# Kernel optimization log

Measured on AMD Instinct MI355X. Metric: run time of the kernel, lower is better.

## Reference

```python
import jax, jax.numpy as jnp
import numpy as np

N_NODES = 50000
N_EDGES = 800000
D = 128          # input_node_dim == output_node_dim (residual)
T = 3            # number of node types == number of edge types
NODE_IN = D + T * D  # node updater input dim = 512


def setup_inputs() -> dict:
    key = jax.random.key(0)
    ks = jax.random.split(key, 8)
    scale = 0.05
    return {
        "node_feature": jax.random.normal(ks[0], (N_NODES, D), jnp.float32),
        "W_e": jax.random.normal(ks[1], (T, D, D), jnp.float32) * scale,
        "b_e": jnp.zeros((T, D), jnp.float32),
        "W_n": jax.random.normal(ks[2], (T, D, NODE_IN), jnp.float32) * scale,
        "b_n": jnp.zeros((T, D), jnp.float32),
        "edge_src": jax.random.randint(ks[3], (N_EDGES,), 0, N_NODES, jnp.int32),
        "edge_dst": jax.random.randint(ks[4], (N_EDGES,), 0, N_NODES, jnp.int32),
        "edge_type": jax.random.randint(ks[5], (N_EDGES,), 0, T, jnp.int32),
        "node_type": jax.random.randint(ks[6], (N_NODES,), 0, T, jnp.int32),
    }


def reference(node_feature, W_e, b_e, W_n, b_n, edge_src, edge_dst, edge_type, node_type):
    N, Din = node_feature.shape
    n_types = W_e.shape[0]
    out_dim = W_e.shape[1]

    # message_function: per-edge-type MLP on source features, relu, zero elsewhere
    src = node_feature[edge_src]                      # [E, D] gather
    parts = [jax.nn.relu(node_feature)]               # reduce_function relu's node_feature
    for t in range(n_types):
        msg = jax.nn.relu(src @ W_e[t].T + b_e[t])    # [E, out]
        msg = jnp.where((edge_type == t)[:, None], msg, jnp.zeros((), msg.dtype))
        # mailbox sum over incoming edges per destination node
        parts.append(jax.ops.segment_sum(msg, edge_dst, num_segments=N))
    agg = jnp.concatenate(parts, axis=1)              # [N, D + T*out]

    # per-node-type updater MLP, dispatched by node_type
    updated = jnp.zeros((N, out_dim), node_feature.dtype)
    for t in range(n_types):
        o = agg @ W_n[t].T + b_n[t]                   # [N, out]
        updated = jnp.where((node_type == t)[:, None], o, updated)

    # use_residual = True
    return updated + node_feature
```

## Files before the change

kernel.cpp:

```cpp
#include <hip/hip_runtime.h>
#include <hip/hip_bf16.h>

#define NN 50000
#define NE 800000
#define DD 128
#define NT 3
#define AGGW 384
#define EM 64
#define EM2 128
#define LDK 136
#define CB 32
#define LDK2 520
#define NBITS 7
#define NBINS ((NN + 127) / 128)
#define EPB 8192
#define BINCAP 2560
#define NTILES_MAX (((NN + EM - 1) / EM) + NT)
#define NTILE_PAD (((NTILES_MAX + 7) / 8) * 8)

typedef __bf16 bf16x8 __attribute__((ext_vector_type(8)));
typedef float f32x4 __attribute__((ext_vector_type(4)));
typedef unsigned short u16x8 __attribute__((ext_vector_type(8)));
typedef unsigned int u32x4 __attribute__((ext_vector_type(4)));

__device__ __forceinline__ unsigned short f2b(float f) {
    __hip_bfloat16 h = __float2bfloat16(f);
    return __builtin_bit_cast(unsigned short, h);
}
__device__ __forceinline__ float b2f(unsigned int u16bits) {
    unsigned int x = u16bits << 16;
    return __builtin_bit_cast(float, x);
}

__global__ void k_prep(const float* __restrict__ nf, const float* __restrict__ We,
                       const float* __restrict__ Wn, unsigned short* __restrict__ nfb,
                       unsigned short* __restrict__ Web, unsigned short* __restrict__ Wnb,
                       int* __restrict__ bhist, int* __restrict__ cnts) {
    size_t i = (size_t)blockIdx.x * blockDim.x + threadIdx.x;
    if (i < NBINS) bhist[i] = 0;
    if (i >= NBINS && i < NBINS + 16) cnts[i - NBINS] = 0;
    const size_t n0 = (size_t)NN * DD / 8;
    const size_t n1 = (size_t)NT * DD * DD / 8;
    const size_t n2 = (size_t)NT * DD * 512 / 8;
    size_t total = n0 + n1 + n2;
    for (size_t p = i; p < total; p += (size_t)gridDim.x * blockDim.x) {
        const float* s; unsigned short* d; size_t off;
        if (p < n0)            { s = nf; d = nfb; off = p; }
        else if (p < n0 + n1)  { s = We; d = Web; off = p - n0; }
        else                   { s = Wn; d = Wnb; off = p - n0 - n1; }
        const float4* f4 = (const float4*)(s + off * 8);
        float4 x = f4[0], y = f4[1];
        u16x8 u = { f2b(x.x), f2b(x.y), f2b(x.z), f2b(x.w),
                    f2b(y.x), f2b(y.y), f2b(y.z), f2b(y.w) };
        *(u16x8*)(d + off * 8) = u;
    }
}

__global__ __launch_bounds__(256) void k_binhist(const int* __restrict__ edst,
        const int* __restrict__ ntp, int* __restrict__ bhist, int* __restrict__ cnts) {
    __shared__ int lh[NBINS];
    __shared__ int ln[3];
    int tid = threadIdx.x;
    for (int i = tid; i < NBINS; i += 256) lh[i] = 0;
    if (tid < 3) ln[tid] = 0;
    __syncthreads();
    int i0 = blockIdx.x * blockDim.x + tid;
    int stride = gridDim.x * blockDim.x;
    for (int p = i0; p < NE; p += stride) atomicAdd(&lh[edst[p] >> NBITS], 1);
    for (int p = i0; p < NN; p += stride) atomicAdd(&ln[ntp[p]], 1);
    __syncthreads();
    for (int i = tid; i < NBINS; i += 256) if (lh[i]) atomicAdd(&bhist[i], lh[i]);
    if (tid < 3) atomicAdd(&cnts[6 + tid], ln[tid]);
}

__global__ __launch_bounds__(512) void k_binscan(const int* __restrict__ bhist,
        int* __restrict__ binptr, int* __restrict__ bincur, int* __restrict__ rowptr) {
    __shared__ int sa[NBINS], sb[NBINS];
    int tid = threadIdx.x;
    if (tid < NBINS) sa[tid] = bhist[tid];
    __syncthreads();
    int flip = 0;
    for (int off = 1; off < NBINS; off <<= 1) {
        int* src = flip ? sb : sa;
        int* dst = flip ? sa : sb;
        if (tid < NBINS) dst[tid] = src[tid] + ((tid >= off) ? src[tid - off] : 0);
        __syncthreads();
        flip ^= 1;
    }
    int* inc = flip ? sb : sa;
    if (tid < NBINS) {
        int excl = (tid == 0) ? 0 : inc[tid - 1];
        binptr[tid] = excl;
        bincur[tid] = excl;
    }
    if (tid == 0) { binptr[NBINS] = NE; rowptr[NN] = NE; }
}

__global__ __launch_bounds__(512) void k_mid(
        const unsigned short* __restrict__ nfb, const unsigned short* __restrict__ Web,
        const float* __restrict__ be, unsigned short* __restrict__ M,
        const int* __restrict__ esrc, const int* __restrict__ edst,
        const int* __restrict__ et, const int* __restrict__ ntp,
        int* __restrict__ bincur, int* __restrict__ cnts,
        int* __restrict__ pe, int* __restrict__ sn, int* __restrict__ rnk) {
    const int NEB = (NE + EPB - 1) / EPB;
    const int NCH2 = (NN + 511) / 512;
    const int TILES = (NN + EM2 - 1) / EM2;
    __shared__ unsigned short Wsm[DD][LDK];
    int tid = threadIdx.x, b = blockIdx.x;

    if (b < NEB) {
        int* lh = (int*)&Wsm[0][0];
        int* gb = lh + NBINS;
        int* lr = gb + NBINS;
        for (int i = tid; i < NBINS; i += 512) { lh[i] = 0; lr[i] = 0; }
        __syncthreads();
        int e0 = b * EPB;
#pragma unroll
        for (int i = 0; i < EPB; i += 512) {
            int e = e0 + i + tid;
            if (e < NE) atomicAdd(&lh[edst[e] >> NBITS], 1);
        }
        __syncthreads();
        for (int i = tid; i < NBINS; i += 512)
            if (lh[i]) gb[i] = atomicAdd(&bincur[i], lh[i]);
        __syncthreads();
#pragma unroll
        for (int i = 0; i < EPB; i += 512) {
            int e = e0 + i + tid;
            if (e < NE) {
                int d = edst[e];
                int t = et[e];
                int bin = d >> NBITS;
                int rank = atomicAdd(&lr[bin], 1);
                pe[gb[bin] + rank] = (t * NN + esrc[e]) | ((d & 127) << 18) | (t << 25);
            }
        }
    } else if (b < NEB + NCH2) {
        int* lcnt = (int*)&Wsm[0][0];
        int* lbase = lcnt + 4;
        if (tid < 3) lcnt[tid] = 0;
        __syncthreads();
        int p = (b - NEB) * 512 + tid;
        int t = -1, rank = 0;
        if (p < NN) { t = ntp[p]; rank = atomicAdd(&lcnt[t], 1); }
        __syncthreads();
        if (tid < 3) lbase[tid] = atomicAdd(&cnts[9 + tid], lcnt[tid]);
        __syncthreads();
        if (p < NN) {
            int c0 = cnts[6], c1 = cnts[7];
            int off = (t == 0) ? 0 : (t == 1) ? c0 : c0 + c1;
            int pos = off + lbase[t] + rank;
            sn[pos] = p;
            rnk[p] = pos;
        }
    } else {
        int bb = b - NEB - NCH2;
        int t = bb / TILES, tile = bb % TILES;
        int base = tile * EM2;
        int m = min(EM2, NN - base);
        {
            int row = tid >> 2, c0 = (tid & 3) * 32;
            const u16x8* src = (const u16x8*)(Web + ((size_t)t * DD + row) * DD + c0);
#pragma unroll
            for (int v = 0; v < 4; ++v) *(u16x8*)&Wsm[row][c0 + v * 8] = src[v];
        }
        __syncthreads();

        int wave = tid >> 6, l = tid & 63, lr2 = l & 15, kg = l >> 4;
        int arow = min(base + wave * 16 + lr2, NN - 1);
        const u16x8* Arow = (const u16x8*)(nfb + (size_t)arow * DD);
        f32x4 acc[8];
#pragma unroll
        for (int n = 0; n < 8; n++) acc[n] = (f32x4){0.f, 0.f, 0.f, 0.f};
#pragma unroll
        for (int k0 = 0; k0 < DD; k0 += 32) {
            bf16x8 a = __builtin_bit_cast(bf16x8, Arow[(k0 >> 3) + kg]);
#pragma unroll
            for (int n = 0; n < 8; n++) {
                bf16x8 bbv = *(const bf16x8*)&Wsm[n * 16 + lr2][k0 + kg * 8];
                acc[n] = __builtin_amdgcn_mfma_f32_16x16x32_bf16(a, bbv, acc[n], 0, 0, 0);
            }
        }
        unsigned short* Mt = M + (size_t)t * NN * DD;
#pragma unroll
        for (int n = 0; n < 8; n++) {
            int col = n * 16 + lr2;
            float bias = be[t * DD + col];
#pragma unroll
            for (int r = 0; r < 4; r++) {
                int row = wave * 16 + kg * 4 + r;
                if (row < m) {
                    float v = acc[n][r] + bias;
                    Mt[(size_t)(base + row) * DD + col] = f2b(fmaxf(v, 0.f));
                }
            }
        }
    }
}

__global__ __launch_bounds__(512) void k_binsort(const int* __restrict__ binptr,
        int* __restrict__ pe, int* __restrict__ rowptr) {
    __shared__ int lcnt[128], lrk[128], lrp[128];
    __shared__ unsigned int sorted[BINCAP];
    int b = blockIdx.x, tid = threadIdx.x;
    int beg = binptr[b], end = binptr[b + 1];
    int cnt = min(end - beg, BINCAP);
    if (tid < 128) { lcnt[tid] = 0; lrk[tid] = 0; }
    __syncthreads();
    for (int e = tid; e < cnt; e += 512)
        atomicAdd(&lcnt[(pe[beg + e] >> 18) & 127], 1);
    __syncthreads();
    if (tid < 64) {
        int v = lcnt[2 * tid] + lcnt[2 * tid + 1];
        int s = v;
        for (int d = 1; d < 64; d <<= 1) {
            int u = __shfl_up(s, d);
            if (tid >= d) s += u;
        }
        int excl = s - v;
        lrp[2 * tid] = excl;
        lrp[2 * tid + 1] = excl + lcnt[2 * tid];
    }
    __syncthreads();
    if (tid < 128) {
        int node = b * 128 + tid;
        if (node < NN) rowptr[node] = beg + lrp[tid];
    }
    for (int e = tid; e < cnt; e += 512) {
        unsigned int p = pe[beg + e];
        int d = (p >> 18) & 127;
        int pos = lrp[d] + atomicAdd(&lrk[d], 1);
        sorted[pos] = p;
    }
    __syncthreads();
    for (int e = tid; e < cnt; e += 512) pe[beg + e] = sorted[e];
}

__global__ __launch_bounds__(128) void k_agg(const unsigned short* __restrict__ M,
        const int* __restrict__ rowptr, const int* __restrict__ pe,
        const int* __restrict__ rnk, unsigned short* __restrict__ aggb) {
    int node = blockIdx.x * 8 + (threadIdx.x >> 4);
    int q = threadIdx.x & 15;
    int beg = rowptr[node], end = rowptr[node + 1];
    const u32x4* Mu4 = (const u32x4*)M;
    float a0[8] = {0,0,0,0,0,0,0,0};
    float a1[8] = {0,0,0,0,0,0,0,0};
    float a2[8] = {0,0,0,0,0,0,0,0};
    int e = beg;
    while (e < end) {
        unsigned int p[8];
        u32x4 v[8];
#pragma unroll
        for (int j = 0; j < 8; ++j) p[j] = pe[min(e + j, end - 1)];
#pragma unroll
        for (int j = 0; j < 8; ++j)
            if (e + j < end) v[j] = Mu4[(size_t)(p[j] & 0x3FFFFu) * 16 + q];
#pragma unroll
        for (int j = 0; j < 8; ++j) {
            if (e + j < end) {
                int t = p[j] >> 25;
                float f0 = b2f(v[j][0] & 0xFFFF), f1 = b2f(v[j][0] >> 16);
                float f2 = b2f(v[j][1] & 0xFFFF), f3 = b2f(v[j][1] >> 16);
                float f4 = b2f(v[j][2] & 0xFFFF), f5 = b2f(v[j][2] >> 16);
                float f6 = b2f(v[j][3] & 0xFFFF), f7 = b2f(v[j][3] >> 16);
                if (t == 0) {
                    a0[0] += f0; a0[1] += f1; a0[2] += f2; a0[3] += f3;
                    a0[4] += f4; a0[5] += f5; a0[6] += f6; a0[7] += f7;
                } else if (t == 1) {
                    a1[0] += f0; a1[1] += f1; a1[2] += f2; a1[3] += f3;
                    a1[4] += f4; a1[5] += f5; a1[6] += f6; a1[7] += f7;
                } else {
                    a2[0] += f0; a2[1] += f1; a2[2] += f2; a2[3] += f3;
                    a2[4] += f4; a2[5] += f5; a2[6] += f6; a2[7] += f7;
                }
            }
        }
        e += 8;
    }
    unsigned int* dst = (unsigned int*)(aggb + (size_t)rnk[node] * AGGW);
    u32x4 o0 = { (unsigned int)f2b(a0[0]) | ((unsigned int)f2b(a0[1]) << 16),
                 (unsigned int)f2b(a0[2]) | ((unsigned int)f2b(a0[3]) << 16),
                 (unsigned int)f2b(a0[4]) | ((unsigned int)f2b(a0[5]) << 16),
                 (unsigned int)f2b(a0[6]) | ((unsigned int)f2b(a0[7]) << 16) };
    u32x4 o1 = { (unsigned int)f2b(a1[0]) | ((unsigned int)f2b(a1[1]) << 16),
                 (unsigned int)f2b(a1[2]) | ((unsigned int)f2b(a1[3]) << 16),
                 (unsigned int)f2b(a1[4]) | ((unsigned int)f2b(a1[5]) << 16),
                 (unsigned int)f2b(a1[6]) | ((unsigned int)f2b(a1[7]) << 16) };
    u32x4 o2 = { (unsigned int)f2b(a2[0]) | ((unsigned int)f2b(a2[1]) << 16),
                 (unsigned int)f2b(a2[2]) | ((unsigned int)f2b(a2[3]) << 16),
                 (unsigned int)f2b(a2[4]) | ((unsigned int)f2b(a2[5]) << 16),
                 (unsigned int)f2b(a2[6]) | ((unsigned int)f2b(a2[7]) << 16) };
    ((u32x4*)dst)[q]        = o0;
    ((u32x4*)(dst + 64))[q] = o1;
    ((u32x4*)(dst + 128))[q] = o2;
}

__global__ __launch_bounds__(256, 3) void k_node(const float* __restrict__ nf,
        const unsigned short* __restrict__ nfb, const unsigned short* __restrict__ Wnb,
        const float* __restrict__ bn, const int* __restrict__ sn,
        const int* __restrict__ cnts, const unsigned short* __restrict__ aggb,
        float* __restrict__ out) {
    __shared__ unsigned short Wsm[CB][LDK2];
    int c0 = cnts[6], c1 = cnts[7], c2 = cnts[8];
    int n0 = (c0 + EM - 1) / EM, n1 = (c1 + EM - 1) / EM, n2 = (c2 + EM - 1) / EM;
    int ntile = n0 + n1 + n2;
    int b = blockIdx.x;
    int rt = (b & 7) * (NTILE_PAD / 8) + (b >> 3);
    if (rt >= ntile) return;
    int tid = threadIdx.x;
    int wave = tid >> 6, l = tid & 63, lr = l & 15, kg = l >> 4;
    int t, tile;
    if (rt < n0) { t = 0; tile = rt; }
    else if (rt < n0 + n1) { t = 1; tile = rt - n0; }
    else { t = 2; tile = rt - n0 - n1; }
    int off = (t == 0) ? 0 : (t == 1) ? c0 : c0 + c1;
    int cntt = (t == 0) ? c0 : (t == 1) ? c1 : c2;
    int base = off + tile * EM;
    int m = min(EM, cntt - tile * EM);

    int srtrow = base + min(wave * 16 + lr, m - 1);
    int myrow = sn[srtrow];
    const u16x8* An = (const u16x8*)(nfb + (size_t)myrow * DD);
    const u16x8* Ag = (const u16x8*)(aggb + (size_t)srtrow * AGGW);
    u16x8 afr[16];
#pragma unroll
    for (int kc = 0; kc < 4; ++kc) {
#pragma unroll
        for (int k0 = 0; k0 < DD; k0 += 32) {
            u16x8 araw;
            if (kc == 0) {
                araw = An[(k0 >> 3) + kg];
#pragma unroll
                for (int j = 0; j < 8; ++j)
                    araw[j] = (araw[j] & 0x8000) ? (unsigned short)0 : araw[j];
            } else {
                araw = Ag[((kc - 1) * DD + k0) / 8 + kg];
            }
            afr[kc * 4 + (k0 >> 5)] = araw;
        }
    }

    int nd[4];
#pragma unroll
    for (int r = 0; r < 4; ++r) nd[r] = sn[base + min(wave * 16 + kg * 4 + r, m - 1)];

    int srow = tid & 31, scc = (tid >> 5) * 64;
#pragma unroll 1
    for (int cbk = 0; cbk < 4; ++cbk) {
        if (cbk) __syncthreads();
        const u16x8* src = (const u16x8*)(Wnb + ((size_t)t * DD + cbk * CB + srow) * 512 + scc);
#pragma unroll
        for (int v = 0; v < 8; ++v) *(u16x8*)&Wsm[srow][scc + v * 8] = src[v];
        __syncthreads();

        f32x4 acc0 = {0.f, 0.f, 0.f, 0.f}, acc1 = {0.f, 0.f, 0.f, 0.f};
#pragma unroll
        for (int kc = 0; kc < 4; ++kc) {
#pragma unroll
            for (int k0 = 0; k0 < DD; k0 += 32) {
                bf16x8 a = __builtin_bit_cast(bf16x8, afr[kc * 4 + (k0 >> 5)]);
                int kw = kc * DD + k0 + kg * 8;
                bf16x8 b0 = *(const bf16x8*)&Wsm[lr][kw];
                bf16x8 b1 = *(const bf16x8*)&Wsm[16 + lr][kw];
                acc0 = __builtin_amdgcn_mfma_f32_16x16x32_bf16(a, b0, acc0, 0, 0, 0);
                acc1 = __builtin_amdgcn_mfma_f32_16x16x32_bf16(a, b1, acc1, 0, 0, 0);
            }
        }
#pragma unroll
        for (int n = 0; n < 2; n++) {
            int col = cbk * CB + n * 16 + lr;
            float bias = bn[t * DD + col];
            const f32x4& av = n ? acc1 : acc0;
#pragma unroll
            for (int r = 0; r < 4; r++) {
                int row = wave * 16 + kg * 4 + r;
                if (row < m) {
                    int node = nd[r];
                    out[(size_t)node * DD + col] = av[r] + bias + nf[(size_t)node * DD + col];
                }
            }
        }
    }
}

extern "C" void kernel_launch(void* const* d_in, const int* in_sizes, int n_in,
                              void* d_out, int out_size, void* d_ws, size_t ws_size,
                              hipStream_t stream) {
    const float* nf   = (const float*)d_in[0];
    const float* We   = (const float*)d_in[1];
    const float* be   = (const float*)d_in[2];
    const float* Wn   = (const float*)d_in[3];
    const float* bn   = (const float*)d_in[4];
    const int*   esrc = (const int*)d_in[5];
    const int*   edst = (const int*)d_in[6];
    const int*   et   = (const int*)d_in[7];
    const int*   ntp  = (const int*)d_in[8];
    float* out = (float*)d_out;

    char* w = (char*)d_ws;
    unsigned short* M    = (unsigned short*)w;  w += (size_t)NT * NN * DD * 2;
    unsigned short* aggb = (unsigned short*)w;  w += (size_t)NN * AGGW * 2;
    unsigned short* nfb  = (unsigned short*)w;  w += (size_t)NN * DD * 2;
    unsigned short* Web  = (unsigned short*)w;  w += (size_t)NT * DD * DD * 2;
    unsigned short* Wnb  = (unsigned short*)w;  w += (size_t)NT * DD * 512 * 2;
    int* pe     = (int*)w;  w += (size_t)NE * 4;
    int* bhist  = (int*)w;  w += (NBINS + 1) * 4;
    int* binptr = (int*)w;  w += (NBINS + 1) * 4;
    int* bincur = (int*)w;  w += (NBINS + 1) * 4;
    int* rowptr = (int*)w;  w += (size_t)(NN + 1) * 4;
    int* sn     = (int*)w;  w += (size_t)NN * 4;
    int* rnk    = (int*)w;  w += (size_t)NN * 4;
    int* cnts   = (int*)w;  w += 16 * 4;

    const int NEB = (NE + EPB - 1) / EPB;
    const int NCH2 = (NN + 511) / 512;
    const int TILES2 = (NN + EM2 - 1) / EM2;

    k_prep<<<1024, 256, 0, stream>>>(nf, We, Wn, nfb, Web, Wnb, bhist, cnts);
    k_binhist<<<256, 256, 0, stream>>>(edst, ntp, bhist, cnts);
    k_binscan<<<1, 512, 0, stream>>>(bhist, binptr, bincur, rowptr);
    k_mid<<<NEB + NCH2 + NT * TILES2, 512, 0, stream>>>(nfb, Web, be, M,
            esrc, edst, et, ntp, bincur, cnts, pe, sn, rnk);
    k_binsort<<<NBINS, 512, 0, stream>>>(binptr, pe, rowptr);
    k_agg<<<NN / 8, 128, 0, stream>>>(M, rowptr, pe, rnk, aggb);
    k_node<<<NTILE_PAD, 256, 0, stream>>>(nf, nfb, Wnb, bn, sn, cnts, aggb, out);
}
```

Baseline: 129.4 us.

## Fuse edge aggregation into node updater kernel via shared-memory tile

```diff
diff --git a/kernel.cpp b/kernel.cpp
--- a/kernel.cpp
+++ b/kernel.cpp
@@ -5,18 +5,17 @@
 #define NE 800000
 #define DD 128
 #define NT 3
-#define AGGW 384
 #define EM 64
 #define EM2 128
 #define LDK 136
 #define CB 32
-#define LDK2 520
 #define NBITS 7
 #define NBINS ((NN + 127) / 128)
 #define EPB 8192
 #define BINCAP 2560
 #define NTILES_MAX (((NN + EM - 1) / EM) + NT)
 #define NTILE_PAD (((NTILES_MAX + 7) / 8) * 8)
+#define AGGP 392
 
 typedef __bf16 bf16x8 __attribute__((ext_vector_type(8)));
 typedef float f32x4 __attribute__((ext_vector_type(4)));
@@ -102,7 +101,7 @@
         const int* __restrict__ esrc, const int* __restrict__ edst,
         const int* __restrict__ et, const int* __restrict__ ntp,
         int* __restrict__ bincur, int* __restrict__ cnts,
-        int* __restrict__ pe, int* __restrict__ sn, int* __restrict__ rnk) {
+        int* __restrict__ pe, int* __restrict__ sn) {
     const int NEB = (NE + EPB - 1) / EPB;
     const int NCH2 = (NN + 511) / 512;
     const int TILES = (NN + EM2 - 1) / EM2;
@@ -150,9 +149,7 @@
         if (p < NN) {
             int c0 = cnts[6], c1 = cnts[7];
             int off = (t == 0) ? 0 : (t == 1) ? c0 : c0 + c1;
-            int pos = off + lbase[t] + rank;
-            sn[pos] = p;
-            rnk[p] = pos;
+            sn[off + lbase[t] + rank] = p;
         }
     } else {
         int bb = b - NEB - NCH2;
@@ -237,71 +234,13 @@
     for (int e = tid; e < cnt; e += 512) pe[beg + e] = sorted[e];
 }
 
-__global__ __launch_bounds__(128) void k_agg(const unsigned short* __restrict__ M,
-        const int* __restrict__ rowptr, const int* __restrict__ pe,
-        const int* __restrict__ rnk, unsigned short* __restrict__ aggb) {
-    int node = blockIdx.x * 8 + (threadIdx.x >> 4);
-    int q = threadIdx.x & 15;
-    int beg = rowptr[node], end = rowptr[node + 1];
-    const u32x4* Mu4 = (const u32x4*)M;
-    float a0[8] = {0,0,0,0,0,0,0,0};
-    float a1[8] = {0,0,0,0,0,0,0,0};
-    float a2[8] = {0,0,0,0,0,0,0,0};
-    int e = beg;
-    while (e < end) {
-        unsigned int p[8];
-        u32x4 v[8];
-#pragma unroll
-        for (int j = 0; j < 8; ++j) p[j] = pe[min(e + j, end - 1)];
-#pragma unroll
-        for (int j = 0; j < 8; ++j)
-            if (e + j < end) v[j] = Mu4[(size_t)(p[j] & 0x3FFFFu) * 16 + q];
-#pragma unroll
-        for (int j = 0; j < 8; ++j) {
-            if (e + j < end) {
-                int t = p[j] >> 25;
-                float f0 = b2f(v[j][0] & 0xFFFF), f1 = b2f(v[j][0] >> 16);
-                float f2 = b2f(v[j][1] & 0xFFFF), f3 = b2f(v[j][1] >> 16);
-                float f4 = b2f(v[j][2] & 0xFFFF), f5 = b2f(v[j][2] >> 16);
-                float f6 = b2f(v[j][3] & 0xFFFF), f7 = b2f(v[j][3] >> 16);
-                if (t == 0) {
-                    a0[0] += f0; a0[1] += f1; a0[2] += f2; a0[3] += f3;
-                    a0[4] += f4; a0[5] += f5; a0[6] += f6; a0[7] += f7;
-                } else if (t == 1) {
-                    a1[0] += f0; a1[1] += f1; a1[2] += f2; a1[3] += f3;
-                    a1[4] += f4; a1[5] += f5; a1[6] += f6; a1[7] += f7;
-                } else {
-                    a2[0] += f0; a2[1] += f1; a2[2] += f2; a2[3] += f3;
-                    a2[4] += f4; a2[5] += f5; a2[6] += f6; a2[7] += f7;
-                }
-            }
-        }
-        e += 8;
-    }
-    unsigned int* dst = (unsigned int*)(aggb + (size_t)rnk[node] * AGGW);
-    u32x4 o0 = { (unsigned int)f2b(a0[0]) | ((unsigned int)f2b(a0[1]) << 16),
-                 (unsigned int)f2b(a0[2]) | ((unsigned int)f2b(a0[3]) << 16),
-                 (unsigned int)f2b(a0[4]) | ((unsigned int)f2b(a0[5]) << 16),
-                 (unsigned int)f2b(a0[6]) | ((unsigned int)f2b(a0[7]) << 16) };
-    u32x4 o1 = { (unsigned int)f2b(a1[0]) | ((unsigned int)f2b(a1[1]) << 16),
-                 (unsigned int)f2b(a1[2]) | ((unsigned int)f2b(a1[3]) << 16),
-                 (unsigned int)f2b(a1[4]) | ((unsigned int)f2b(a1[5]) << 16),
-                 (unsigned int)f2b(a1[6]) | ((unsigned int)f2b(a1[7]) << 16) };
-    u32x4 o2 = { (unsigned int)f2b(a2[0]) | ((unsigned int)f2b(a2[1]) << 16),
-                 (unsigned int)f2b(a2[2]) | ((unsigned int)f2b(a2[3]) << 16),
-                 (unsigned int)f2b(a2[4]) | ((unsigned int)f2b(a2[5]) << 16),
-                 (unsigned int)f2b(a2[6]) | ((unsigned int)f2b(a2[7]) << 16) };
-    ((u32x4*)dst)[q]        = o0;
-    ((u32x4*)(dst + 64))[q] = o1;
-    ((u32x4*)(dst + 128))[q] = o2;
-}
-
-__global__ __launch_bounds__(256, 3) void k_node(const float* __restrict__ nf,
+__global__ __launch_bounds__(256, 3) void k_fuse(const float* __restrict__ nf,
         const unsigned short* __restrict__ nfb, const unsigned short* __restrict__ Wnb,
         const float* __restrict__ bn, const int* __restrict__ sn,
-        const int* __restrict__ cnts, const unsigned short* __restrict__ aggb,
+        const int* __restrict__ cnts, const int* __restrict__ rowptr,
+        const int* __restrict__ pe, const unsigned short* __restrict__ M,
         float* __restrict__ out) {
-    __shared__ unsigned short Wsm[CB][LDK2];
+    __shared__ unsigned short agg[EM][AGGP];
     int c0 = cnts[6], c1 = cnts[7], c2 = cnts[8];
     int n0 = (c0 + EM - 1) / EM, n1 = (c1 + EM - 1) / EM, n2 = (c2 + EM - 1) / EM;
     int ntile = n0 + n1 + n2;
@@ -309,7 +248,7 @@
     int rt = (b & 7) * (NTILE_PAD / 8) + (b >> 3);
     if (rt >= ntile) return;
     int tid = threadIdx.x;
-    int wave = tid >> 6, l = tid & 63, lr = l & 15, kg = l >> 4;
+    int wave = tid >> 6, l = tid & 63;
     int t, tile;
     if (rt < n0) { t = 0; tile = rt; }
     else if (rt < n0 + n1) { t = 1; tile = rt - n0; }
@@ -319,50 +258,105 @@
     int base = off + tile * EM;
     int m = min(EM, cntt - tile * EM);
 
-    int srtrow = base + min(wave * 16 + lr, m - 1);
-    int myrow = sn[srtrow];
+    {
+        int g = l >> 4, q = l & 15;
+        const u32x4* Mu4 = (const u32x4*)M;
+#pragma unroll 1
+        for (int j = 0; j < 4; ++j) {
+            int rloc = wave * 16 + g * 4 + j;
+            if (rloc >= m) break;
+            int node = sn[base + rloc];
+            int beg = rowptr[node], end = rowptr[node + 1];
+            float a0[8] = {0,0,0,0,0,0,0,0};
+            float a1[8] = {0,0,0,0,0,0,0,0};
+            float a2[8] = {0,0,0,0,0,0,0,0};
+            int e = beg;
+            while (e < end) {
+                unsigned int p[8];
+                u32x4 v[8];
+#pragma unroll
+                for (int jj = 0; jj < 8; ++jj) p[jj] = pe[min(e + jj, end - 1)];
+#pragma unroll
+                for (int jj = 0; jj < 8; ++jj)
+                    if (e + jj < end) v[jj] = Mu4[(size_t)(p[jj] & 0x3FFFFu) * 16 + q];
+#pragma unroll
+                for (int jj = 0; jj < 8; ++jj) {
+                    if (e + jj < end) {
+                        int tt = p[jj] >> 25;
+                        float f0 = b2f(v[jj][0] & 0xFFFF), f1 = b2f(v[jj][0] >> 16);
+                        float f2 = b2f(v[jj][1] & 0xFFFF), f3 = b2f(v[jj][1] >> 16);
+                        float f4 = b2f(v[jj][2] & 0xFFFF), f5 = b2f(v[jj][2] >> 16);
+                        float f6 = b2f(v[jj][3] & 0xFFFF), f7 = b2f(v[jj][3] >> 16);
+                        if (tt == 0) {
+                            a0[0] += f0; a0[1] += f1; a0[2] += f2; a0[3] += f3;
+                            a0[4] += f4; a0[5] += f5; a0[6] += f6; a0[7] += f7;
+                        } else if (tt == 1) {
+                            a1[0] += f0; a1[1] += f1; a1[2] += f2; a1[3] += f3;
+                            a1[4] += f4; a1[5] += f5; a1[6] += f6; a1[7] += f7;
+                        } else {
+                            a2[0] += f0; a2[1] += f1; a2[2] += f2; a2[3] += f3;
+                            a2[4] += f4; a2[5] += f5; a2[6] += f6; a2[7] += f7;
+                        }
+                    }
+                }
+                e += 8;
+            }
+            u32x4 o0 = { (unsigned int)f2b(a0[0]) | ((unsigned int)f2b(a0[1]) << 16),
+                         (unsigned int)f2b(a0[2]) | ((unsigned int)f2b(a0[3]) << 16),
+                         (unsigned int)f2b(a0[4]) | ((unsigned int)f2b(a0[5]) << 16),
+                         (unsigned int)f2b(a0[6]) | ((unsigned int)f2b(a0[7]) << 16) };
+            u32x4 o1 = { (unsigned int)f2b(a1[0]) | ((unsigned int)f2b(a1[1]) << 16),
+                         (unsigned int)f2b(a1[2]) | ((unsigned int)f2b(a1[3]) << 16),
+                         (unsigned int)f2b(a1[4]) | ((unsigned int)f2b(a1[5]) << 16),
+                         (unsigned int)f2b(a1[6]) | ((unsigned int)f2b(a1[7]) << 16) };
+            u32x4 o2 = { (unsigned int)f2b(a2[0]) | ((unsigned int)f2b(a2[1]) << 16),
+                         (unsigned int)f2b(a2[2]) | ((unsigned int)f2b(a2[3]) << 16),
+                         (unsigned int)f2b(a2[4]) | ((unsigned int)f2b(a2[5]) << 16),
+                         (unsigned int)f2b(a2[6]) | ((unsigned int)f2b(a2[7]) << 16) };
+            *(u32x4*)&agg[rloc][q * 8]       = o0;
+            *(u32x4*)&agg[rloc][128 + q * 8] = o1;
+            *(u32x4*)&agg[rloc][256 + q * 8] = o2;
+        }
+    }
+    asm volatile("s_waitcnt lgkmcnt(0)" ::: "memory");
+
+    int lr = l & 15, kg = l >> 4;
+    int myrow = sn[base + min(wave * 16 + lr, m - 1)];
     const u16x8* An = (const u16x8*)(nfb + (size_t)myrow * DD);
-    const u16x8* Ag = (const u16x8*)(aggb + (size_t)srtrow * AGGW);
     u16x8 afr[16];
 #pragma unroll
-    for (int kc = 0; kc < 4; ++kc) {
-#pragma unroll
-        for (int k0 = 0; k0 < DD; k0 += 32) {
-            u16x8 araw;
-            if (kc == 0) {
-                araw = An[(k0 >> 3) + kg];
-#pragma unroll
-                for (int j = 0; j < 8; ++j)
-                    araw[j] = (araw[j] & 0x8000) ? (unsigned short)0 : araw[j];
-            } else {
-                araw = Ag[((kc - 1) * DD + k0) / 8 + kg];
-            }
-            afr[kc * 4 + (k0 >> 5)] = araw;
-        }
-    }
+    for (int k0 = 0; k0 < DD; k0 += 32) {
+        u16x8 araw = An[(k0 >> 3) + kg];
+#pragma unroll
+        for (int jj = 0; jj < 8; ++jj)
+            araw[jj] = (araw[jj] & 0x8000) ? (unsigned short)0 : araw[jj];
+        afr[k0 >> 5] = araw;
+    }
+#pragma unroll
+    for (int kc = 1; kc < 4; ++kc)
+#pragma unroll
+        for (int k0 = 0; k0 < DD; k0 += 32)
+            afr[kc * 4 + (k0 >> 5)] =
+                *(const u16x8*)&agg[wave * 16 + lr][(kc - 1) * DD + k0 + kg * 8];
 
     int nd[4];
 #pragma unroll
     for (int r = 0; r < 4; ++r) nd[r] = sn[base + min(wave * 16 + kg * 4 + r, m - 1)];
 
-    int srow = tid & 31, scc = (tid >> 5) * 64;
+    const u16x8* W0 = (const u16x8*)(Wnb + ((size_t)t * DD + lr) * 512);
+    const u16x8* W1 = (const u16x8*)(Wnb + ((size_t)t * DD + 16 + lr) * 512);
 #pragma unroll 1
     for (int cbk = 0; cbk < 4; ++cbk) {
-        if (cbk) __syncthreads();
-        const u16x8* src = (const u16x8*)(Wnb + ((size_t)t * DD + cbk * CB + srow) * 512 + scc);
-#pragma unroll
-        for (int v = 0; v < 8; ++v) *(u16x8*)&Wsm[srow][scc + v * 8] = src[v];
-        __syncthreads();
-
         f32x4 acc0 = {0.f, 0.f, 0.f, 0.f}, acc1 = {0.f, 0.f, 0.f, 0.f};
+        size_t crow = (size_t)cbk * CB * 512 / 8;
 #pragma unroll
         for (int kc = 0; kc < 4; ++kc) {
 #pragma unroll
             for (int k0 = 0; k0 < DD; k0 += 32) {
                 bf16x8 a = __builtin_bit_cast(bf16x8, afr[kc * 4 + (k0 >> 5)]);
-                int kw = kc * DD + k0 + kg * 8;
-                bf16x8 b0 = *(const bf16x8*)&Wsm[lr][kw];
-                bf16x8 b1 = *(const bf16x8*)&Wsm[16 + lr][kw];
+                int kwo = (kc * DD + k0 + kg * 8) >> 3;
+                bf16x8 b0 = __builtin_bit_cast(bf16x8, W0[crow + kwo]);
+                bf16x8 b1 = __builtin_bit_cast(bf16x8, W1[crow + kwo]);
                 acc0 = __builtin_amdgcn_mfma_f32_16x16x32_bf16(a, b0, acc0, 0, 0, 0);
                 acc1 = __builtin_amdgcn_mfma_f32_16x16x32_bf16(a, b1, acc1, 0, 0, 0);
             }
@@ -400,7 +394,6 @@
 
     char* w = (char*)d_ws;
     unsigned short* M    = (unsigned short*)w;  w += (size_t)NT * NN * DD * 2;
-    unsigned short* aggb = (unsigned short*)w;  w += (size_t)NN * AGGW * 2;
     unsigned short* nfb  = (unsigned short*)w;  w += (size_t)NN * DD * 2;
     unsigned short* Web  = (unsigned short*)w;  w += (size_t)NT * DD * DD * 2;
     unsigned short* Wnb  = (unsigned short*)w;  w += (size_t)NT * DD * 512 * 2;
@@ -410,7 +403,6 @@
     int* bincur = (int*)w;  w += (NBINS + 1) * 4;
     int* rowptr = (int*)w;  w += (size_t)(NN + 1) * 4;
     int* sn     = (int*)w;  w += (size_t)NN * 4;
-    int* rnk    = (int*)w;  w += (size_t)NN * 4;
     int* cnts   = (int*)w;  w += 16 * 4;
 
     const int NEB = (NE + EPB - 1) / EPB;
@@ -421,8 +413,7 @@
     k_binhist<<<256, 256, 0, stream>>>(edst, ntp, bhist, cnts);
     k_binscan<<<1, 512, 0, stream>>>(bhist, binptr, bincur, rowptr);
     k_mid<<<NEB + NCH2 + NT * TILES2, 512, 0, stream>>>(nfb, Web, be, M,
-            esrc, edst, et, ntp, bincur, cnts, pe, sn, rnk);
+            esrc, edst, et, ntp, bincur, cnts, pe, sn);
     k_binsort<<<NBINS, 512, 0, stream>>>(binptr, pe, rowptr);
-    k_agg<<<NN / 8, 128, 0, stream>>>(M, rowptr, pe, rnk, aggb);
-    k_node<<<NTILE_PAD, 256, 0, stream>>>(nf, nfb, Wnb, bn, sn, cnts, aggb, out);
-}
+    k_fuse<<<NTILE_PAD, 256, 0, stream>>>(nf, nfb, Wnb, bn, sn, cnts, rowptr, pe, M, out);
+}
```

After: 174.5 us. 1.35x slower.
